# Kernel tuning notes

Hardware: AMD Instinct MI355X
Metric: run time of the kernel (lower is better)

Reference implementation:

```python
import jax, jax.numpy as jnp
import numpy as np

B, L, D, H = 4, 1024, 768, 6
DH = D // H
EPS = 1e-5


def setup_inputs() -> dict:
    key = jax.random.key(0)
    kq, kk, kv, kl, kw = jax.random.split(key, 5)
    Q = jax.random.normal(kq, (B, L, D), jnp.float32)
    K = jax.random.normal(kk, (B, L, D), jnp.float32)
    V = jax.random.normal(kv, (B, L, D), jnp.float32)
    # realistic padding: each batch element has a valid length in [L//2, L]
    lengths = jax.random.randint(kl, (B,), L // 2, L + 1)
    valid = jnp.arange(L)[None, :] < lengths[:, None]          # (B, L)
    pad_mask = valid[:, :, None] & valid[:, None, :]           # (B, L, L), True = keep
    bx_packed = ~valid                                         # (B, L), True = padded
    # BatchNorm affine params (per-head channels)
    g1 = jnp.ones((H,), jnp.float32)
    b1 = jnp.zeros((H,), jnp.float32)
    g2 = jnp.ones((H,), jnp.float32)
    b2 = jnp.zeros((H,), jnp.float32)
    # posterior gate: Linear(H, 2)
    Wp = jax.random.normal(kw, (2, H), jnp.float32) * (1.0 / np.sqrt(H))
    bp = jnp.zeros((2,), jnp.float32)
    return {"Q": Q, "K": K, "V": V, "pad_mask": pad_mask, "bx_packed": bx_packed,
            "g1": g1, "b1": b1, "g2": g2, "b2": b2, "Wp": Wp, "bp": bp}


def _split_heads(x):
    b, l, _ = x.shape
    return x.reshape(b, l, H, DH).transpose(0, 2, 1, 3)  # (B, H, L, DH)


def _batchnorm(x, g, b):
    # x: (B, H, N); training-mode BatchNorm1d over channels H (stats over B and N)
    m = x.mean(axis=(0, 2), keepdims=True)
    v = x.var(axis=(0, 2), keepdims=True)  # biased, as torch uses for normalization
    return (x - m) * jax.lax.rsqrt(v + EPS) * g[None, :, None] + b[None, :, None]


def _remove_nan(x):
    return jnp.where(jnp.isnan(x), jnp.zeros_like(x), x)


def reference(Q, K, V, pad_mask, bx_packed, g1, b1, g2, b2, Wp, bp):
    Qh, Kh, Vh = _split_heads(Q), _split_heads(K), _split_heads(V)
    b, h, l, _ = Qh.shape
    # DistMatrix: negative squared Euclidean distance between query/key vectors
    # scores[b,h,i,j] = -||Q_i - K_j||^2, via the GEMM-friendly expansion
    q2 = jnp.sum(Qh * Qh, axis=-1)                     # (B, H, L)
    k2 = jnp.sum(Kh * Kh, axis=-1)                     # (B, H, L)
    qk = jnp.einsum("bhid,bhjd->bhij", Qh, Kh)         # (B, H, L, L)
    co = -(q2[..., :, None] + k2[..., None, :] - 2.0 * qk)
    # norm1 over flattened L*L
    co = _batchnorm(co.reshape(b, h, l * l), g1, b1).reshape(b, h, l, l)
    # zero out positions where pad_mask is False (in-place masked fill in torch)
    co = jnp.where(pad_mask[:, None, :, :], co, 0.0)
    co = jax.nn.softmax(co, axis=-1)
    co = _remove_nan(co)
    # column-sum attention mass per key position
    w = co.sum(axis=-2)                                # (B, H, L)
    w = _batchnorm(w, g2, b2).transpose(0, 2, 1)       # (B, L, H)
    # posterior gate: Linear(H,2) + softmax, take class-0 probability
    w = jax.nn.softmax(w @ Wp.T + bp, axis=-1)[..., 0]  # (B, L)
    w = _remove_nan(w)
    w = jnp.where(bx_packed, -jnp.inf, w)
    w = jax.nn.softmax(w, axis=-1)
    w = _remove_nan(w)[..., None]                      # (B, L, 1)
    return co, w, Vh
```

## Files before the change

### kernel.cpp

```cpp
#include <hip/hip_runtime.h>
#include <stdint.h>
#include <stddef.h>

#define BB 4
#define LL 1024
#define DD 768
#define HH 6
#define DHH 128
#define EPS 1e-5f
#define LOG2E 1.44269504088896f

#define CO_ELEMS 25165824
#define W_ELEMS  4096

#define OFF_Q2  0
#define OFF_K2  24576
#define OFF_WC  49152
#define OFF_SP  73728
#define OFF_AC  79872
#define OFF_SS  79888
#define OFF_WP  81920
#define OFF_GP  1654784
#define OFF_MS1 5193728
#define OFF_MS2 5242880
#define OFF_CT  5292032

typedef __attribute__((ext_vector_type(8))) short short8;
typedef __attribute__((ext_vector_type(4))) float f32x4;

__device__ __forceinline__ short8 ld_bf8(const float* __restrict__ p) {
    const float4 a = *(const float4*)(p);
    const float4 b = *(const float4*)(p + 4);
    short8 r;
    r[0] = (short)(__float_as_uint(a.x) >> 16);
    r[1] = (short)(__float_as_uint(a.y) >> 16);
    r[2] = (short)(__float_as_uint(a.z) >> 16);
    r[3] = (short)(__float_as_uint(a.w) >> 16);
    r[4] = (short)(__float_as_uint(b.x) >> 16);
    r[5] = (short)(__float_as_uint(b.y) >> 16);
    r[6] = (short)(__float_as_uint(b.z) >> 16);
    r[7] = (short)(__float_as_uint(b.w) >> 16);
    return r;
}

__device__ __forceinline__ short8 pack_bf8(float4 a, float4 b) {
    short8 r;
    r[0] = (short)(__float_as_uint(a.x) >> 16);
    r[1] = (short)(__float_as_uint(a.y) >> 16);
    r[2] = (short)(__float_as_uint(a.z) >> 16);
    r[3] = (short)(__float_as_uint(a.w) >> 16);
    r[4] = (short)(__float_as_uint(b.x) >> 16);
    r[5] = (short)(__float_as_uint(b.y) >> 16);
    r[6] = (short)(__float_as_uint(b.z) >> 16);
    r[7] = (short)(__float_as_uint(b.w) >> 16);
    return r;
}

__global__ __launch_bounds__(256) void k_gram(
        const float* __restrict__ Q, const float* __restrict__ K,
        const float* __restrict__ V,
        float* __restrict__ ws, float* __restrict__ gramP,
        float* __restrict__ ms1, float* __restrict__ ms2,
        float* __restrict__ vh, unsigned* __restrict__ ctr) {
    const int ic = blockIdx.x;
    const int bh = blockIdx.y;
    const int which = blockIdx.z;
    const int b = bh / HH, h = bh - b * HH;
    const int t = threadIdx.x;

    if (which == 2) {
        if (ic == 0 && bh == 0 && t < 32) ctr[t] = 0u;
        const float* srcv = V + (size_t)b * LL * DD + h * DHH;
        float* dstv = vh + ((size_t)bh * LL + (size_t)ic * 128) * DHH;
#pragma unroll
        for (int p = 0; p < 16; p++) {
            const int idx = p * 256 + t;
            const int row = idx >> 5, d4 = idx & 31;
            f32x4 v = *(const f32x4*)(srcv + (size_t)(ic * 128 + row) * DD + d4 * 4);
            __builtin_nontemporal_store(v, (f32x4*)(dstv + (size_t)row * DHH + d4 * 4));
        }
        return;
    }

    const float* src = (which ? K : Q) + (size_t)b * LL * DD + h * DHH;
    float* sqout = ws + (which ? OFF_K2 : OFF_Q2) + bh * 1024 + ic * 128;

    const int lane = t & 63, wv = t >> 6;
    const int lm = lane & 15, quad = lane >> 4;

    __shared__ float tileT[128][129];
    __shared__ float q2loc[128];

    const int ig = t >> 5;
    const int d0 = (t & 31) * 4;
#pragma unroll 4
    for (int p = 0; p < 16; p++) {
        const int i_loc = p * 8 + ig;
        float4 v = *(const float4*)(src + (size_t)(ic * 128 + i_loc) * DD + d0);
        tileT[d0 + 0][i_loc] = __uint_as_float(__float_as_uint(v.x) & 0xffff0000u);
        tileT[d0 + 1][i_loc] = __uint_as_float(__float_as_uint(v.y) & 0xffff0000u);
        tileT[d0 + 2][i_loc] = __uint_as_float(__float_as_uint(v.z) & 0xffff0000u);
        tileT[d0 + 3][i_loc] = __uint_as_float(__float_as_uint(v.w) & 0xffff0000u);
        float s = v.x * v.x + v.y * v.y + v.z * v.z + v.w * v.w;
#pragma unroll
        for (int off = 1; off < 32; off <<= 1) s += __shfl_xor(s, off);
        if ((t & 31) == 0) { q2loc[i_loc] = s; sqout[i_loc] = s; }
    }
    __syncthreads();

    if (t < 128) {
        float s1 = 0.f, s2 = 0.f;
#pragma unroll 8
        for (int i = 0; i < 128; i++) {
            float v = tileT[t][i];
            s1 += v;
            s2 += v * q2loc[i];
        }
        const size_t mo = ((size_t)(which * 24 + bh) * 8 + ic) * 128 + t;
        ms1[mo] = s1;
        ms2[mo] = s2;
    }

    const size_t gbase = ((size_t)(which * 24 + bh) * 8 + ic) * 9216;
    int pi = 0;
    for (int dt = 0; dt < 8; dt++) {
        for (int et = dt; et < 8; et++, pi++) {
            if ((pi & 3) != wv) continue;
            f32x4 acc = (f32x4)(0.0f);
#pragma unroll
            for (int kk = 0; kk < 4; kk++) {
                const int i0 = kk * 32 + quad * 8;
                const float* pa = &tileT[dt * 16 + lm][i0];
                const float* pb = &tileT[et * 16 + lm][i0];
                short8 af, bf;
#pragma unroll
                for (int e = 0; e < 8; e++) {
                    af[e] = (short)(__float_as_uint(pa[e]) >> 16);
                    bf[e] = (short)(__float_as_uint(pb[e]) >> 16);
                }
                acc = __builtin_amdgcn_mfma_f32_16x16x32_bf16(af, bf, acc, 0, 0, 0);
            }
            if (dt != et && which == 0) {
                acc[0] *= 2.f; acc[1] *= 2.f; acc[2] *= 2.f; acc[3] *= 2.f;
            }
            *(f32x4*)&gramP[gbase + (size_t)pi * 256 + lane * 4] = acc;
        }
    }
}

__global__ __launch_bounds__(1024) void k_stats3(
        const float* __restrict__ ms1, const float* __restrict__ ms2,
        const float* __restrict__ gramP,
        const float* __restrict__ q2, const float* __restrict__ k2,
        const float* __restrict__ g1, const float* __restrict__ b1,
        float* __restrict__ statsP, float* __restrict__ ac,
        unsigned* __restrict__ ctr) {
    const int bh = blockIdx.x;
    const int t = threadIdx.x, lane = t & 63, w = t >> 6;
    __shared__ float sQ[128], sK[128], sQq2[128], sKk2[128];
    __shared__ float sred[16][4];
    __shared__ float gred[16];

    if (t < 256) {
        const int d = t & 127, which = t >> 7;
        const float* p1 = ms1 + (size_t)(which * 24 + bh) * 1024 + d;
        const float* p2 = ms2 + (size_t)(which * 24 + bh) * 1024 + d;
        float s1 = 0.f, s2 = 0.f;
#pragma unroll
        for (int ic = 0; ic < 8; ic++) { s1 += p1[ic * 128]; s2 += p2[ic * 128]; }
        if (which) { sK[d] = s1; sKk2[d] = s2; }
        else       { sQ[d] = s1; sQq2[d] = s2; }
    }
    if (t >= 512 && t < 768) {
        const int tt = t - 512;
        f32x4 qv = *(const f32x4*)(q2 + bh * 1024 + tt * 4);
        f32x4 kv = *(const f32x4*)(k2 + bh * 1024 + tt * 4);
        float p0 = qv[0] + qv[1] + qv[2] + qv[3];
        float p1 = qv[0]*qv[0] + qv[1]*qv[1] + qv[2]*qv[2] + qv[3]*qv[3];
        float p2 = kv[0] + kv[1] + kv[2] + kv[3];
        float p3 = kv[0]*kv[0] + kv[1]*kv[1] + kv[2]*kv[2] + kv[3]*kv[3];
#pragma unroll
        for (int off = 1; off < 64; off <<= 1) {
            p0 += __shfl_xor(p0, off); p1 += __shfl_xor(p1, off);
            p2 += __shfl_xor(p2, off); p3 += __shfl_xor(p3, off);
        }
        if (lane == 0) { sred[w][0] = p0; sred[w][1] = p1; sred[w][2] = p2; sred[w][3] = p3; }
    }
    {
        const float* gq = gramP + (size_t)(0 * 24 + bh) * 8 * 9216;
        const float* gk = gramP + (size_t)(1 * 24 + bh) * 8 * 9216;
        float gg = 0.f;
#pragma unroll
        for (int it = 0; it < 9; it++) {
            const int f = it * 1024 + t;
            float a = 0.f, c = 0.f;
#pragma unroll
            for (int icc = 0; icc < 8; icc++) {
                a += gq[(size_t)icc * 9216 + f];
                c += gk[(size_t)icc * 9216 + f];
            }
            gg += a * c;
        }
#pragma unroll
        for (int off = 1; off < 64; off <<= 1) gg += __shfl_xor(gg, off);
        if (lane == 0) gred[w] = gg;
    }
    __syncthreads();
    if (t < 64) {
        float dA  = sQ[t] * sK[t] + sQ[t + 64] * sK[t + 64];
        float dBq = sQq2[t] * sK[t] + sQq2[t + 64] * sK[t + 64];
        float dBk = sQ[t] * sKk2[t] + sQ[t + 64] * sKk2[t + 64];
#pragma unroll
        for (int off = 1; off < 64; off <<= 1) {
            dA += __shfl_xor(dA, off); dBq += __shfl_xor(dBq, off); dBk += __shfl_xor(dBk, off);
        }
        if (t == 0) {
            float SQ2   = sred[8][0] + sred[9][0] + sred[10][0] + sred[11][0];
            float SQ2SQ = sred[8][1] + sred[9][1] + sred[10][1] + sred[11][1];
            float SK2   = sred[8][2] + sred[9][2] + sred[10][2] + sred[11][2];
            float SK2SQ = sred[8][3] + sred[9][3] + sred[10][3] + sred[11][3];
            float GG = 0.f;
#pragma unroll
            for (int i = 0; i < 16; i++) GG += gred[i];
            float sumS  = 2.f * dA - 1024.f * (SQ2 + SK2);
            float sumS2 = 4.f * GG + 1024.f * (SQ2SQ + SK2SQ) + 2.f * SQ2 * SK2 - 4.f * (dBq + dBk);
            statsP[bh * 2]     = sumS;
            statsP[bh * 2 + 1] = sumS2;
            __threadfence();
            unsigned old = atomicAdd(&ctr[30], 1u);
            if (old == 23u) {
                __threadfence();
#pragma unroll
                for (int h = 0; h < HH; h++) {
                    float T1 = 0.f, T2 = 0.f;
#pragma unroll
                    for (int b = 0; b < 4; b++) {
                        T1 += statsP[(b * HH + h) * 2];
                        T2 += statsP[(b * HH + h) * 2 + 1];
                    }
                    const float N = 4194304.f;
                    float m_ = T1 / N;
                    float var = fmaxf(T2 / N - m_ * m_, 0.0f);
                    float r = rsqrtf(var + EPS);
                    float a = r * g1[h];
                    ac[h] = a;
                    ac[8 + h] = b1[h] - m_ * a;
                }
            }
        }
    }
}

#define KLOAD(buf, jtv) do {                                                   \
    const float* _p = Kb + (size_t)(jw + (jtv) * 16 + lm) * DD + quad * 8;     \
    buf##0 = *(const float4*)(_p);        buf##1 = *(const float4*)(_p + 4);   \
    buf##2 = *(const float4*)(_p + 32);   buf##3 = *(const float4*)(_p + 36);  \
    buf##4 = *(const float4*)(_p + 64);   buf##5 = *(const float4*)(_p + 68);  \
    buf##6 = *(const float4*)(_p + 96);   buf##7 = *(const float4*)(_p + 100); \
} while (0)

#define KCOMP(buf, jtv) do {                                                   \
    short8 kf0 = pack_bf8(buf##0, buf##1);                                     \
    short8 kf1 = pack_bf8(buf##2, buf##3);                                     \
    short8 kf2 = pack_bf8(buf##4, buf##5);                                     \
    short8 kf3 = pack_bf8(buf##6, buf##7);                                     \
    f32x4 acc0 = (f32x4)(0.0f), acc1 = (f32x4)(0.0f);                          \
    acc0 = __builtin_amdgcn_mfma_f32_16x16x32_bf16(kf0, qf[0][0], acc0, 0, 0, 0); \
    acc1 = __builtin_amdgcn_mfma_f32_16x16x32_bf16(kf0, qf[1][0], acc1, 0, 0, 0); \
    acc0 = __builtin_amdgcn_mfma_f32_16x16x32_bf16(kf1, qf[0][1], acc0, 0, 0, 0); \
    acc1 = __builtin_amdgcn_mfma_f32_16x16x32_bf16(kf1, qf[1][1], acc1, 0, 0, 0); \
    acc0 = __builtin_amdgcn_mfma_f32_16x16x32_bf16(kf2, qf[0][2], acc0, 0, 0, 0); \
    acc1 = __builtin_amdgcn_mfma_f32_16x16x32_bf16(kf2, qf[1][2], acc1, 0, 0, 0); \
    acc0 = __builtin_amdgcn_mfma_f32_16x16x32_bf16(kf3, qf[0][3], acc0, 0, 0, 0); \
    acc1 = __builtin_amdgcn_mfma_f32_16x16x32_bf16(kf3, qf[1][3], acc1, 0, 0, 0); \
    const int jb = jw + (jtv) * 16;                                            \
    const f32x4 k2v = *(const f32x4*)(k2b + jb + quad * 4);                    \
    const uchar4 m4 = *(const uchar4*)(bxb + jb + quad * 4);                   \
    const bool vj0 = (m4.x == 0), vj1 = (m4.y == 0);                           \
    const bool vj2 = (m4.z == 0), vj3 = (m4.w == 0);                           \
    f32x4 kc;                                                                  \
    kc[0] = a1l * k2v[0]; kc[1] = a1l * k2v[1];                                \
    kc[2] = a1l * k2v[2]; kc[3] = a1l * k2v[3];                                \
    {                                                                          \
        f32x4 ev;                                                              \
        ev[0] = (vi0 && vj0) ? exp2f(fminf(fmaf(a2l, acc0[0], cr0 - kc[0]), 86.56f)) : 1.0f; \
        ev[1] = (vi0 && vj1) ? exp2f(fminf(fmaf(a2l, acc0[1], cr0 - kc[1]), 86.56f)) : 1.0f; \
        ev[2] = (vi0 && vj2) ? exp2f(fminf(fmaf(a2l, acc0[2], cr0 - kc[2]), 86.56f)) : 1.0f; \
        ev[3] = (vi0 && vj3) ? exp2f(fminf(fmaf(a2l, acc0[3], cr0 - kc[3]), 86.56f)) : 1.0f; \
        *(f32x4*)&e_lds[lm][jb + quad * 4] = ev;                               \
        rsum0 += (ev[0] + ev[1]) + (ev[2] + ev[3]);                            \
    }                                                                          \
    {                                                                          \
        f32x4 ev;                                                              \
        ev[0] = (vi1 && vj0) ? exp2f(fminf(fmaf(a2l, acc1[0], cr1 - kc[0]), 86.56f)) : 1.0f; \
        ev[1] = (vi1 && vj1) ? exp2f(fminf(fmaf(a2l, acc1[1], cr1 - kc[1]), 86.56f)) : 1.0f; \
        ev[2] = (vi1 && vj2) ? exp2f(fminf(fmaf(a2l, acc1[2], cr1 - kc[2]), 86.56f)) : 1.0f; \
        ev[3] = (vi1 && vj3) ? exp2f(fminf(fmaf(a2l, acc1[3], cr1 - kc[3]), 86.56f)) : 1.0f; \
        *(f32x4*)&e_lds[16 + lm][jb + quad * 4] = ev;                          \
        rsum1 += (ev[0] + ev[1]) + (ev[2] + ev[3]);                            \
    }                                                                          \
} while (0)

__global__ __launch_bounds__(512, 1) void k_fused(
        const float* __restrict__ Q, const float* __restrict__ Km,
        const float* __restrict__ q2, const float* __restrict__ k2,
        const float* __restrict__ ac, const unsigned char* __restrict__ bx,
        const float* __restrict__ g2, const float* __restrict__ b2,
        const float* __restrict__ Wp, const float* __restrict__ bp,
        float* __restrict__ co, float* __restrict__ wcolP,
        float* __restrict__ wcol, float* __restrict__ ws2,
        unsigned* __restrict__ ctr, float* __restrict__ wout) {
    const int g = blockIdx.x;
    const int xcd = g & 7, slot = g >> 3;
    const int t = threadIdx.x, lane = t & 63, w = t >> 6;
    const int lm = lane & 15, quad = lane >> 4;
    const int jw = w * 128;

    __shared__ float e_lds[32][1028];
    __shared__ float rowsum[3][32];
    __shared__ int sclaim[2];
    __shared__ int stail;
    __shared__ float scr[8][2];
    __shared__ float abuf[12];
    if (t < 96) ((float*)rowsum)[t] = 0.f;
    __syncthreads();

#pragma unroll 1
    for (int rep = 0; rep < 3; rep++) {
        const int idx = slot * 3 + rep;
        const int bh = xcd + ((idx >> 5) << 3);
        const int strip = idx & 31;
        const int b = bh / HH, h = bh - b * HH;
        const int i0 = strip * 32;
        const float* Qb = Q + (size_t)b * LL * DD + h * DHH;
        const float* Kb = Km + (size_t)b * LL * DD + h * DHH;
        const float* k2b = k2 + bh * 1024;
        const unsigned char* bxb = bx + b * LL;
        const float a1l = ac[h] * LOG2E;
        const float a2l = 2.0f * a1l;
        const float c1l = ac[8 + h] * LOG2E;

        short8 qf[2][4];
#pragma unroll
        for (int s = 0; s < 2; s++)
#pragma unroll
            for (int kk = 0; kk < 4; kk++)
                qf[s][kk] = ld_bf8(Qb + (size_t)(i0 + s * 16 + lm) * DD + kk * 32 + quad * 8);

        const bool vi0 = (bxb[i0 + lm] == 0);
        const bool vi1 = (bxb[i0 + 16 + lm] == 0);
        const float cr0 = c1l - a1l * q2[bh * 1024 + i0 + lm];
        const float cr1 = c1l - a1l * q2[bh * 1024 + i0 + 16 + lm];

        float4 rA0, rA1, rA2, rA3, rA4, rA5, rA6, rA7;
        float4 rB0, rB1, rB2, rB3, rB4, rB5, rB6, rB7;

        float rsum0 = 0.f, rsum1 = 0.f;
        KLOAD(rA, 0);
        KLOAD(rB, 1);
        KCOMP(rA, 0);
        KLOAD(rA, 2);
        KCOMP(rB, 1);
        KLOAD(rB, 3);
        KCOMP(rA, 2);
        KLOAD(rA, 4);
        KCOMP(rB, 3);
        KLOAD(rB, 5);
        KCOMP(rA, 4);
        KLOAD(rA, 6);
        KCOMP(rB, 5);
        KLOAD(rB, 7);
        KCOMP(rA, 6);
        KCOMP(rB, 7);

        rsum0 += __shfl_xor(rsum0, 16);
        rsum0 += __shfl_xor(rsum0, 32);
        rsum1 += __shfl_xor(rsum1, 16);
        rsum1 += __shfl_xor(rsum1, 32);
        if (lane < 16) {
            atomicAdd(&rowsum[rep][lm], rsum0);
            atomicAdd(&rowsum[rep][16 + lm], rsum1);
        }
        __syncthreads();

        const int cg = t & 255, rh = t >> 8;
        float* cob = co + ((size_t)bh << 20) + (size_t)(i0 + rh * 16) * 1024 + cg * 4;
        float* wp = wcolP + ((size_t)((strip * 2 + rh) * 24 + bh)) * 1024 + cg * 4;
        float cs0 = 0.f, cs1 = 0.f, cs2 = 0.f, cs3 = 0.f;
#pragma unroll
        for (int rr = 0; rr < 16; rr++) {
            const int r = rh * 16 + rr;
            const float inv = 1.0f / rowsum[rep][r];
            f32x4 v = *(const f32x4*)&e_lds[r][cg * 4];
            v[0] *= inv; v[1] *= inv; v[2] *= inv; v[3] *= inv;
            __builtin_nontemporal_store(v, (f32x4*)(cob + (size_t)rr * 1024));
            cs0 += v[0]; cs1 += v[1]; cs2 += v[2]; cs3 += v[3];
        }
        f32x4 wv; wv[0] = cs0; wv[1] = cs1; wv[2] = cs2; wv[3] = cs3;
        *(f32x4*)wp = wv;
        __syncthreads();
    }

    asm volatile("s_waitcnt vmcnt(0)" ::: "memory");
    __threadfence();
    __syncthreads();
    if (t == 0) {
        sclaim[0] = -1; sclaim[1] = -1; stail = 0;
        int nc = 0;
#pragma unroll
        for (int r = 0; r < 3; r++) {
            const int idxv = slot * 3 + r;
            const int bhv = xcd + ((idxv >> 5) << 3);
            unsigned o = atomicAdd(&ctr[bhv], 1u);
            if (o == 31u) sclaim[nc++] = bhv;
        }
    }
    __syncthreads();
    const int ncl = (sclaim[0] >= 0) + (sclaim[1] >= 0);
    if (ncl) {
        __threadfence();
        for (int c = 0; c < 2; c++) {
            const int cb = sclaim[c];
            if (cb < 0) continue;
            const int c0 = t, c1 = t + 512;
            float s0 = 0.f, s1 = 0.f;
            for (int sp = 0; sp < 64; sp++) {
                const float* wp_ = wcolP + ((size_t)sp * 24 + cb) * 1024;
                s0 += wp_[c0];
                s1 += wp_[c1];
            }
            wcol[cb * 1024 + c0] = s0;
            wcol[cb * 1024 + c1] = s1;
            float a = s0 + s1, q = s0 * s0 + s1 * s1;
#pragma unroll
            for (int off = 1; off < 64; off <<= 1) { a += __shfl_xor(a, off); q += __shfl_xor(q, off); }
            if (lane == 0) { scr[w][0] = a; scr[w][1] = q; }
            __syncthreads();
            if (t == 0) {
                float A = 0.f, Qq = 0.f;
#pragma unroll
                for (int i = 0; i < 8; i++) { A += scr[i][0]; Qq += scr[i][1]; }
                ws2[cb * 2] = A; ws2[cb * 2 + 1] = Qq;
            }
            __syncthreads();
        }
        asm volatile("s_waitcnt vmcnt(0)" ::: "memory");
        __threadfence();
    }
    __syncthreads();
    if (t == 0 && ncl) {
        int tc = 0;
#pragma unroll
        for (int c = 0; c < 2; c++)
            if (sclaim[c] >= 0) {
                unsigned o = atomicAdd(&ctr[24], 1u);
                if (o == 23u) tc = 1;
            }
        stail = tc;
    }
    __syncthreads();
    if (stail) {
        __threadfence();
        if (t < HH) {
            float s = 0.f, s2 = 0.f;
#pragma unroll
            for (int b_ = 0; b_ < 4; b_++) {
                s  += ws2[(b_ * HH + t) * 2];
                s2 += ws2[(b_ * HH + t) * 2 + 1];
            }
            float m = s / 4096.f;
            float var = fmaxf(s2 / 4096.f - m * m, 0.0f);
            float r = rsqrtf(var + EPS);
            float a = r * g2[t];
            abuf[t] = a;
            abuf[6 + t] = b2[t] - m * a;
        }
        __syncthreads();
        if (w < 4) {
            const int b_ = w;
            const float bp0 = bp[0], bp1 = bp[1];
            float vbuf[16];
            float mx = -INFINITY;
#pragma unroll
            for (int u = 0; u < 16; u++) {
                const int l = lane * 16 + u;
                float z0 = bp0, z1 = bp1;
#pragma unroll
                for (int h_ = 0; h_ < HH; h_++) {
                    const float wn = abuf[h_] * wcol[(b_ * HH + h_) * 1024 + l] + abuf[6 + h_];
                    z0 += wn * Wp[h_];
                    z1 += wn * Wp[HH + h_];
                }
                const float pc = 1.0f / (1.0f + __expf(z1 - z0));
                const float v_ = bx[b_ * LL + l] ? -INFINITY : pc;
                vbuf[u] = v_;
                mx = fmaxf(mx, v_);
            }
#pragma unroll
            for (int off = 1; off < 64; off <<= 1) mx = fmaxf(mx, __shfl_xor(mx, off));
            float ssum = 0.f;
#pragma unroll
            for (int u = 0; u < 16; u++) { vbuf[u] = __expf(vbuf[u] - mx); ssum += vbuf[u]; }
#pragma unroll
            for (int off = 1; off < 64; off <<= 1) ssum += __shfl_xor(ssum, off);
            const float inv_ = 1.0f / ssum;
#pragma unroll
            for (int u4 = 0; u4 < 4; u4++) {
                f32x4 o;
                o[0] = vbuf[u4 * 4 + 0] * inv_;
                o[1] = vbuf[u4 * 4 + 1] * inv_;
                o[2] = vbuf[u4 * 4 + 2] * inv_;
                o[3] = vbuf[u4 * 4 + 3] * inv_;
                *(f32x4*)&wout[b_ * 1024 + lane * 16 + u4 * 4] = o;
            }
        }
    }
}

extern "C" void kernel_launch(void* const* d_in, const int* in_sizes, int n_in,
                              void* d_out, int out_size, void* d_ws, size_t ws_size,
                              hipStream_t stream) {
    const float* Q  = (const float*)d_in[0];
    const float* K  = (const float*)d_in[1];
    const float* V  = (const float*)d_in[2];
    const unsigned char* bx = (const unsigned char*)d_in[4];
    const float* g1 = (const float*)d_in[5];
    const float* b1 = (const float*)d_in[6];
    const float* g2 = (const float*)d_in[7];
    const float* b2 = (const float*)d_in[8];
    const float* Wp = (const float*)d_in[9];
    const float* bp = (const float*)d_in[10];

    float* out  = (float*)d_out;
    float* co   = out;
    float* wout = out + CO_ELEMS;
    float* vh   = out + CO_ELEMS + W_ELEMS;

    float* ws = (float*)d_ws;
    float* q2     = ws + OFF_Q2;
    float* k2     = ws + OFF_K2;
    float* wcol   = ws + OFF_WC;
    float* statsP = ws + OFF_SP;
    float* ac     = ws + OFF_AC;
    float* ws2    = ws + OFF_SS;
    float* wcolP  = ws + OFF_WP;
    float* gramP  = ws + OFF_GP;
    float* ms1    = ws + OFF_MS1;
    float* ms2    = ws + OFF_MS2;
    unsigned* ctr = (unsigned*)(ws + OFF_CT);

    k_gram<<<dim3(8, 24, 3), 256, 0, stream>>>(Q, K, V, ws, gramP, ms1, ms2, vh, ctr);
    k_stats3<<<24, 1024, 0, stream>>>(ms1, ms2, gramP, q2, k2, g1, b1, statsP, ac, ctr);
    k_fused<<<256, 512, 0, stream>>>(Q, K, q2, k2, ac, bx, g2, b2, Wp, bp,
                                     co, wcolP, wcol, ws2, ctr, wout);
}
```

Before: 322.8 us.

## Split column-sum tail into separate kernel and vectorize gram LDS reads

```diff
diff --git a/kernel.cpp b/kernel.cpp
--- a/kernel.cpp
+++ b/kernel.cpp
@@ -56,6 +56,19 @@
     return r;
 }
 
+__device__ __forceinline__ short8 pack_bf8v(f32x4 a, f32x4 b) {
+    short8 r;
+    r[0] = (short)(__float_as_uint(a[0]) >> 16);
+    r[1] = (short)(__float_as_uint(a[1]) >> 16);
+    r[2] = (short)(__float_as_uint(a[2]) >> 16);
+    r[3] = (short)(__float_as_uint(a[3]) >> 16);
+    r[4] = (short)(__float_as_uint(b[0]) >> 16);
+    r[5] = (short)(__float_as_uint(b[1]) >> 16);
+    r[6] = (short)(__float_as_uint(b[2]) >> 16);
+    r[7] = (short)(__float_as_uint(b[3]) >> 16);
+    return r;
+}
+
 __global__ __launch_bounds__(256) void k_gram(
         const float* __restrict__ Q, const float* __restrict__ K,
         const float* __restrict__ V,
@@ -88,7 +101,7 @@
     const int lane = t & 63, wv = t >> 6;
     const int lm = lane & 15, quad = lane >> 4;
 
-    __shared__ float tileT[128][129];
+    __shared__ float tileT[128][132];
     __shared__ float q2loc[128];
 
     const int ig = t >> 5;
@@ -132,12 +145,8 @@
                 const int i0 = kk * 32 + quad * 8;
                 const float* pa = &tileT[dt * 16 + lm][i0];
                 const float* pb = &tileT[et * 16 + lm][i0];
-                short8 af, bf;
-#pragma unroll
-                for (int e = 0; e < 8; e++) {
-                    af[e] = (short)(__float_as_uint(pa[e]) >> 16);
-                    bf[e] = (short)(__float_as_uint(pb[e]) >> 16);
-                }
+                short8 af = pack_bf8v(*(const f32x4*)pa, *(const f32x4*)(pa + 4));
+                short8 bf = pack_bf8v(*(const f32x4*)pb, *(const f32x4*)(pb + 4));
                 acc = __builtin_amdgcn_mfma_f32_16x16x32_bf16(af, bf, acc, 0, 0, 0);
             }
             if (dt != et && which == 0) {
@@ -305,11 +314,7 @@
         const float* __restrict__ Q, const float* __restrict__ Km,
         const float* __restrict__ q2, const float* __restrict__ k2,
         const float* __restrict__ ac, const unsigned char* __restrict__ bx,
-        const float* __restrict__ g2, const float* __restrict__ b2,
-        const float* __restrict__ Wp, const float* __restrict__ bp,
-        float* __restrict__ co, float* __restrict__ wcolP,
-        float* __restrict__ wcol, float* __restrict__ ws2,
-        unsigned* __restrict__ ctr, float* __restrict__ wout) {
+        float* __restrict__ co, float* __restrict__ wcolP) {
     const int g = blockIdx.x;
     const int xcd = g & 7, slot = g >> 3;
     const int t = threadIdx.x, lane = t & 63, w = t >> 6;
@@ -318,10 +323,6 @@
 
     __shared__ float e_lds[32][1028];
     __shared__ float rowsum[3][32];
-    __shared__ int sclaim[2];
-    __shared__ int stail;
-    __shared__ float scr[8][2];
-    __shared__ float abuf[12];
     if (t < 96) ((float*)rowsum)[t] = 0.f;
     __syncthreads();
 
@@ -400,119 +401,102 @@
         *(f32x4*)wp = wv;
         __syncthreads();
     }
-
+}
+
+__global__ __launch_bounds__(256) void k_wtail(
+        const float* __restrict__ wcolP, float* __restrict__ wcol,
+        float* __restrict__ ws2, unsigned* __restrict__ ctr,
+        const unsigned char* __restrict__ bx,
+        const float* __restrict__ g2, const float* __restrict__ b2,
+        const float* __restrict__ Wp, const float* __restrict__ bp,
+        float* __restrict__ wout) {
+    const int t = threadIdx.x, lane = t & 63, w = t >> 6;
+    __shared__ float sc[4][2];
+    __shared__ int stail;
+    __shared__ float abuf[12];
+
+    const int g = blockIdx.x * 256 + t;
+    float s = 0.f;
+#pragma unroll 8
+    for (int strip = 0; strip < 64; strip++)
+        s += wcolP[(size_t)strip * 24576 + g];
+    wcol[g] = s;
+    float a = s, b = s * s;
+#pragma unroll
+    for (int off = 1; off < 64; off <<= 1) { a += __shfl_xor(a, off); b += __shfl_xor(b, off); }
+    if (lane == 0) { sc[w][0] = a; sc[w][1] = b; }
+    __syncthreads();
+    if (t == 0) {
+        ws2[blockIdx.x * 2]     = sc[0][0] + sc[1][0] + sc[2][0] + sc[3][0];
+        ws2[blockIdx.x * 2 + 1] = sc[0][1] + sc[1][1] + sc[2][1] + sc[3][1];
+    }
     asm volatile("s_waitcnt vmcnt(0)" ::: "memory");
     __threadfence();
     __syncthreads();
     if (t == 0) {
-        sclaim[0] = -1; sclaim[1] = -1; stail = 0;
-        int nc = 0;
-#pragma unroll
-        for (int r = 0; r < 3; r++) {
-            const int idxv = slot * 3 + r;
-            const int bhv = xcd + ((idxv >> 5) << 3);
-            unsigned o = atomicAdd(&ctr[bhv], 1u);
-            if (o == 31u) sclaim[nc++] = bhv;
-        }
-    }
-    __syncthreads();
-    const int ncl = (sclaim[0] >= 0) + (sclaim[1] >= 0);
-    if (ncl) {
-        __threadfence();
-        for (int c = 0; c < 2; c++) {
-            const int cb = sclaim[c];
-            if (cb < 0) continue;
-            const int c0 = t, c1 = t + 512;
-            float s0 = 0.f, s1 = 0.f;
-            for (int sp = 0; sp < 64; sp++) {
-                const float* wp_ = wcolP + ((size_t)sp * 24 + cb) * 1024;
-                s0 += wp_[c0];
-                s1 += wp_[c1];
+        unsigned o = atomicAdd(&ctr[25], 1u);
+        stail = (o == 95u) ? 1 : 0;
+    }
+    __syncthreads();
+    if (!stail) return;
+
+    __threadfence();
+    if (t < HH) {
+        float ss = 0.f, ss2 = 0.f;
+#pragma unroll
+        for (int b_ = 0; b_ < 4; b_++) {
+            const int bh = b_ * HH + t;
+#pragma unroll
+            for (int sub = 0; sub < 4; sub++) {
+                const int blk = bh * 4 + sub;
+                ss  += ws2[blk * 2];
+                ss2 += ws2[blk * 2 + 1];
             }
-            wcol[cb * 1024 + c0] = s0;
-            wcol[cb * 1024 + c1] = s1;
-            float a = s0 + s1, q = s0 * s0 + s1 * s1;
-#pragma unroll
-            for (int off = 1; off < 64; off <<= 1) { a += __shfl_xor(a, off); q += __shfl_xor(q, off); }
-            if (lane == 0) { scr[w][0] = a; scr[w][1] = q; }
-            __syncthreads();
-            if (t == 0) {
-                float A = 0.f, Qq = 0.f;
-#pragma unroll
-                for (int i = 0; i < 8; i++) { A += scr[i][0]; Qq += scr[i][1]; }
-                ws2[cb * 2] = A; ws2[cb * 2 + 1] = Qq;
+        }
+        float m = ss / 4096.f;
+        float var = fmaxf(ss2 / 4096.f - m * m, 0.0f);
+        float r = rsqrtf(var + EPS);
+        float aa = r * g2[t];
+        abuf[t] = aa;
+        abuf[6 + t] = b2[t] - m * aa;
+    }
+    __syncthreads();
+    if (w < 4) {
+        const int b_ = w;
+        const float bp0 = bp[0], bp1 = bp[1];
+        float vbuf[16];
+        float mx = -INFINITY;
+#pragma unroll
+        for (int u = 0; u < 16; u++) {
+            const int l = lane * 16 + u;
+            float z0 = bp0, z1 = bp1;
+#pragma unroll
+            for (int h_ = 0; h_ < HH; h_++) {
+                const float wn = abuf[h_] * wcol[(b_ * HH + h_) * 1024 + l] + abuf[6 + h_];
+                z0 += wn * Wp[h_];
+                z1 += wn * Wp[HH + h_];
             }
-            __syncthreads();
-        }
-        asm volatile("s_waitcnt vmcnt(0)" ::: "memory");
-        __threadfence();
-    }
-    __syncthreads();
-    if (t == 0 && ncl) {
-        int tc = 0;
-#pragma unroll
-        for (int c = 0; c < 2; c++)
-            if (sclaim[c] >= 0) {
-                unsigned o = atomicAdd(&ctr[24], 1u);
-                if (o == 23u) tc = 1;
-            }
-        stail = tc;
-    }
-    __syncthreads();
-    if (stail) {
-        __threadfence();
-        if (t < HH) {
-            float s = 0.f, s2 = 0.f;
-#pragma unroll
-            for (int b_ = 0; b_ < 4; b_++) {
-                s  += ws2[(b_ * HH + t) * 2];
-                s2 += ws2[(b_ * HH + t) * 2 + 1];
-            }
-            float m = s / 4096.f;
-            float var = fmaxf(s2 / 4096.f - m * m, 0.0f);
-            float r = rsqrtf(var + EPS);
-            float a = r * g2[t];
-            abuf[t] = a;
-            abuf[6 + t] = b2[t] - m * a;
-        }
-        __syncthreads();
-        if (w < 4) {
-            const int b_ = w;
-            const float bp0 = bp[0], bp1 = bp[1];
-            float vbuf[16];
-            float mx = -INFINITY;
-#pragma unroll
-            for (int u = 0; u < 16; u++) {
-                const int l = lane * 16 + u;
-                float z0 = bp0, z1 = bp1;
-#pragma unroll
-                for (int h_ = 0; h_ < HH; h_++) {
-                    const float wn = abuf[h_] * wcol[(b_ * HH + h_) * 1024 + l] + abuf[6 + h_];
-                    z0 += wn * Wp[h_];
-                    z1 += wn * Wp[HH + h_];
-                }
-                const float pc = 1.0f / (1.0f + __expf(z1 - z0));
-                const float v_ = bx[b_ * LL + l] ? -INFINITY : pc;
-                vbuf[u] = v_;
-                mx = fmaxf(mx, v_);
-            }
-#pragma unroll
-            for (int off = 1; off < 64; off <<= 1) mx = fmaxf(mx, __shfl_xor(mx, off));
-            float ssum = 0.f;
-#pragma unroll
-            for (int u = 0; u < 16; u++) { vbuf[u] = __expf(vbuf[u] - mx); ssum += vbuf[u]; }
-#pragma unroll
-            for (int off = 1; off < 64; off <<= 1) ssum += __shfl_xor(ssum, off);
-            const float inv_ = 1.0f / ssum;
-#pragma unroll
-            for (int u4 = 0; u4 < 4; u4++) {
-                f32x4 o;
-                o[0] = vbuf[u4 * 4 + 0] * inv_;
-                o[1] = vbuf[u4 * 4 + 1] * inv_;
-                o[2] = vbuf[u4 * 4 + 2] * inv_;
-                o[3] = vbuf[u4 * 4 + 3] * inv_;
-                *(f32x4*)&wout[b_ * 1024 + lane * 16 + u4 * 4] = o;
-            }
+            const float pc = 1.0f / (1.0f + __expf(z1 - z0));
+            const float v_ = bx[b_ * LL + l] ? -INFINITY : pc;
+            vbuf[u] = v_;
+            mx = fmaxf(mx, v_);
+        }
+#pragma unroll
+        for (int off = 1; off < 64; off <<= 1) mx = fmaxf(mx, __shfl_xor(mx, off));
+        float ssum = 0.f;
+#pragma unroll
+        for (int u = 0; u < 16; u++) { vbuf[u] = __expf(vbuf[u] - mx); ssum += vbuf[u]; }
+#pragma unroll
+        for (int off = 1; off < 64; off <<= 1) ssum += __shfl_xor(ssum, off);
+        const float inv_ = 1.0f / ssum;
+#pragma unroll
+        for (int u4 = 0; u4 < 4; u4++) {
+            f32x4 o;
+            o[0] = vbuf[u4 * 4 + 0] * inv_;
+            o[1] = vbuf[u4 * 4 + 1] * inv_;
+            o[2] = vbuf[u4 * 4 + 2] * inv_;
+            o[3] = vbuf[u4 * 4 + 3] * inv_;
+            *(f32x4*)&wout[b_ * 1024 + lane * 16 + u4 * 4] = o;
         }
     }
 }
@@ -551,6 +535,6 @@
 
     k_gram<<<dim3(8, 24, 3), 256, 0, stream>>>(Q, K, V, ws, gramP, ms1, ms2, vh, ctr);
     k_stats3<<<24, 1024, 0, stream>>>(ms1, ms2, gramP, q2, k2, g1, b1, statsP, ac, ctr);
-    k_fused<<<256, 512, 0, stream>>>(Q, K, q2, k2, ac, bx, g2, b2, Wp, bp,
-                                     co, wcolP, wcol, ws2, ctr, wout);
-}
+    k_fused<<<256, 512, 0, stream>>>(Q, K, q2, k2, ac, bx, co, wcolP);
+    k_wtail<<<96, 256, 0, stream>>>(wcolP, wcol, ws2, ctr, bx, g2, b2, Wp, bp, wout);
+}
```

Measured after the change: 272.6 us. 1.18x faster.
